# Optimization experiments

Measured on AMD Instinct MI355X. Metric: run time of the kernel, lower is better.

Reference implementation:

```python
import jax, jax.numpy as jnp
import numpy as np

N_HEAD = 16
SPARSE_TOPK = 64
NEG_INF = float('-inf')


def setup_inputs() -> dict:
    key = jax.random.key(0)
    ks = jax.random.split(key, 12)
    B, T, C = 4, 1024, 1024
    s = 0.02
    q = jax.random.normal(ks[0], (B, T, C), jnp.float32)
    kv = jax.random.normal(ks[1], (B, T, C), jnp.float32)  # forward asserts k == v
    tgt_mask = jnp.tril(jnp.ones((T, T), jnp.bool_)).reshape(1, 1, T, T)
    inp = {'q': q, 'k': kv, 'v': kv, 'tgt_mask': tgt_mask}
    for i, n in enumerate(['Wq', 'Wk', 'Wv', 'Wo']):
        inp[n] = jax.random.normal(ks[2 + i], (C, C), jnp.float32) * s
    for i, n in enumerate(['bq', 'bk', 'bv', 'bo']):
        inp[n] = jax.random.normal(ks[6 + i], (C,), jnp.float32) * s
    return inp


def reference(q, k, v, tgt_mask, Wq, Wk, Wv, Wo, bq, bk, bv, bo):
    B, T, C = q.shape
    H = N_HEAD
    hd = C // H
    scale = 1.0 / np.sqrt(hd).astype(np.float32)
    # QKV projections -> [B, H, T, hd]
    qh = (q @ Wq + bq).reshape(B, T, H, hd).transpose(0, 2, 1, 3)
    kh = (k @ Wk + bk).reshape(B, T, H, hd).transpose(0, 2, 1, 3)
    vh = (v @ Wv + bv).reshape(B, T, H, hd).transpose(0, 2, 1, 3)
    # full attention scores [B, H, T, T]
    att = jnp.einsum('bhtd,bhsd->bhts', qh, kh) * scale
    # causal mask: masked_fill where tgt_mask == 0
    att = jnp.where(tgt_mask[:, :, :T, :T], att, NEG_INF)
    # top-k sparse pruning: keep entries >= k-th largest per row (ties kept)
    top, _ = jax.lax.top_k(att, SPARSE_TOPK)
    vk = top[..., -1:]  # [B, H, T, 1]
    att = jnp.where(att < vk, NEG_INF, att)
    att = jax.nn.softmax(att, axis=-1)
    # dropout is identity in eval (p=0.0)
    y = jnp.einsum('bhts,bhsd->bhtd', att, vh)
    y = y.transpose(0, 2, 1, 3).reshape(B, T, C)
    return y @ Wo + bo
```

## Files before the change

kernel.cpp:

```cpp
#include <hip/hip_runtime.h>
#include <hip/hip_bf16.h>
#include <math.h>

typedef __attribute__((ext_vector_type(8))) short short8;
typedef __attribute__((ext_vector_type(4))) float f32x4;
typedef __attribute__((ext_vector_type(4))) int int4v;

#define SCL 0.1803368801111204f

static __device__ __forceinline__ unsigned short f2bf(float f) {
  unsigned u = __float_as_uint(f);
  u = u + 0x7FFFu + ((u >> 16) & 1u);
  return (unsigned short)(u >> 16);
}

static __device__ __forceinline__ unsigned keyof(float x) {
  unsigned u = __float_as_uint(x);
  return (u & 0x80000000u) ? ~u : (u | 0x80000000u);
}
static __device__ __forceinline__ float keyinv(unsigned k) {
  unsigned u = (k & 0x80000000u) ? (k & 0x7FFFFFFFu) : ~k;
  return __uint_as_float(u);
}

static __device__ __forceinline__ int saddr(int r, int cc) {
  return (((r << 9) + cc) << 2) ^ ((r & 7) << 4);
}
static __device__ __forceinline__ int paddr(int r, int c) {
  return ((r << 11) + (c << 1)) ^ ((r & 7) << 4);
}

static __device__ __forceinline__ void gld_lds16(const unsigned short* g, unsigned short* l) {
  __builtin_amdgcn_global_load_lds(
      (const __attribute__((address_space(1))) void*)g,
      (__attribute__((address_space(3))) void*)l, 16, 0, 0);
}

__global__ __launch_bounds__(256) void cvt3_k(const float* __restrict__ q,
                                              const float* __restrict__ k,
                                              const float* __restrict__ v,
                                              unsigned short* __restrict__ oq,
                                              unsigned short* __restrict__ ok,
                                              unsigned short* __restrict__ ov) {
  const int y = blockIdx.y;
  const float* in = (y == 0) ? q : (y == 1) ? k : v;
  unsigned short* out = (y == 0) ? oq : (y == 1) ? ok : ov;
  const int i = blockIdx.x * 256 + threadIdx.x;
  const f32x4* p = (const f32x4*)in + 2 * (size_t)i;
  f32x4 a = p[0], b = p[1];
  short8 r;
  r[0] = (short)f2bf(a[0]); r[1] = (short)f2bf(a[1]);
  r[2] = (short)f2bf(a[2]); r[3] = (short)f2bf(a[3]);
  r[4] = (short)f2bf(b[0]); r[5] = (short)f2bf(b[1]);
  r[6] = (short)f2bf(b[2]); r[7] = (short)f2bf(b[3]);
  ((short8*)out)[i] = r;
}

__global__ __launch_bounds__(256) void wtrans4_k(const float* __restrict__ Wq,
                                                 const float* __restrict__ Wk,
                                                 const float* __restrict__ Wv,
                                                 const float* __restrict__ Wo,
                                                 unsigned short* __restrict__ Wqt,
                                                 unsigned short* __restrict__ Wkt,
                                                 unsigned short* __restrict__ Wvt,
                                                 unsigned short* __restrict__ Wot) {
  const int z = blockIdx.z;
  const float* W = (z == 0) ? Wq : (z == 1) ? Wk : (z == 2) ? Wv : Wo;
  unsigned short* Wt = (z == 0) ? Wqt : (z == 1) ? Wkt : (z == 2) ? Wvt : Wot;
  __shared__ float tile[32][33];
  const int tx = threadIdx.x, ty = threadIdx.y;
  const int x0 = blockIdx.x * 32, y0 = blockIdx.y * 32;
#pragma unroll
  for (int j = 0; j < 4; ++j)
    tile[ty + j * 8][tx] = W[(y0 + ty + j * 8) * 1024 + x0 + tx];
  __syncthreads();
#pragma unroll
  for (int j = 0; j < 4; ++j)
    Wt[(x0 + ty + j * 8) * 1024 + (y0 + tx)] = f2bf(tile[tx][ty + j * 8]);
}

template <int MODE>
static __device__ __forceinline__ void gemm_body(unsigned short* As0, unsigned short* Bs0,
                                                 unsigned short* As1, unsigned short* Bs1,
                                                 const unsigned short* __restrict__ A,
                                                 const unsigned short* __restrict__ Bt,
                                                 const float* __restrict__ bias,
                                                 void* __restrict__ out) {
  const int tid = threadIdx.x;
  const int lane = tid & 63, w = tid >> 6;
  const int wr = w >> 1, wc = w & 1;
  const int m0 = blockIdx.y * 128, n0 = blockIdx.x * 128;
  const int l15 = lane & 15, l4 = lane >> 4;
  f32x4 acc[4][4] = {};
  const int r0 = tid >> 2, s0 = (tid & 3) * 8;
  const int r1 = r0 + 64;
  const unsigned short* gA0 = A + (m0 + r0) * 1024 + s0;
  const unsigned short* gA1 = A + (m0 + r1) * 1024 + s0;
  const unsigned short* gB0 = Bt + (n0 + r0) * 1024 + s0;
  const unsigned short* gB1 = Bt + (n0 + r1) * 1024 + s0;
  const int oA0 = r0 * 32 + s0, oA1 = r1 * 32 + s0;

  gld_lds16(gA0, As0 + oA0);
  gld_lds16(gA1, As0 + oA1);
  gld_lds16(gB0, Bs0 + oA0);
  gld_lds16(gB1, Bs0 + oA1);
  __syncthreads();

  for (int kt = 0; kt < 32; ++kt) {
    if (kt < 31) {
      const int k0n = (kt + 1) * 32;
      unsigned short* Asn = (kt & 1) ? As0 : As1;
      unsigned short* Bsn = (kt & 1) ? Bs0 : Bs1;
      gld_lds16(gA0 + k0n, Asn + oA0);
      gld_lds16(gA1 + k0n, Asn + oA1);
      gld_lds16(gB0 + k0n, Bsn + oA0);
      gld_lds16(gB1 + k0n, Bsn + oA1);
    }
    const unsigned short* Asc = (kt & 1) ? As1 : As0;
    const unsigned short* Bsc = (kt & 1) ? Bs1 : Bs0;
    short8 af[4], bfr[4];
#pragma unroll
    for (int i = 0; i < 4; ++i) {
      af[i]  = *(const short8*)(Asc + (wr * 64 + i * 16 + l15) * 32 + l4 * 8);
      bfr[i] = *(const short8*)(Bsc + (wc * 64 + i * 16 + l15) * 32 + l4 * 8);
    }
#pragma unroll
    for (int i = 0; i < 4; ++i)
#pragma unroll
      for (int j = 0; j < 4; ++j)
        acc[i][j] = __builtin_amdgcn_mfma_f32_16x16x32_bf16(af[i], bfr[j], acc[i][j], 0, 0, 0);
    __syncthreads();
  }
#pragma unroll
  for (int i = 0; i < 4; ++i) {
#pragma unroll
    for (int j = 0; j < 4; ++j) {
      const int n = n0 + wc * 64 + j * 16 + l15;
      const float bv = bias[n];
#pragma unroll
      for (int r = 0; r < 4; ++r) {
        const int m = m0 + wr * 64 + i * 16 + l4 * 4 + r;
        const float v = acc[i][j][r] + bv;
        if (MODE == 2) {
          ((float*)out)[m * 1024 + n] = v;
        } else {
          const int bb = m >> 10, t = m & 1023, hh = n >> 6, dd = n & 63;
          const unsigned short bfv = f2bf(v);
          if (MODE == 0)
            ((unsigned short*)out)[(((bb << 4) + hh) * 1024 + t) * 64 + dd] = bfv;
          else
            ((unsigned short*)out)[(((bb << 4) + hh) * 64 + dd) * 1024 + t] = bfv;
        }
      }
    }
  }
}

__global__ __launch_bounds__(256) void gemm_qkv_k(
    const unsigned short* qbf, const unsigned short* kbf, const unsigned short* vbf,
    const unsigned short* Wqt, const unsigned short* Wkt, const unsigned short* Wvt,
    const float* bq, const float* bk, const float* bv,
    unsigned short* Qh, unsigned short* Kh, unsigned short* Vth) {
  __shared__ unsigned short As0[128 * 32], Bs0[128 * 32], As1[128 * 32], Bs1[128 * 32];
  const int z = blockIdx.z;
  const unsigned short* A  = (z == 0) ? qbf : ((z == 1) ? kbf : vbf);
  const unsigned short* Bt = (z == 0) ? Wqt : ((z == 1) ? Wkt : Wvt);
  const float* bias        = (z == 0) ? bq  : ((z == 1) ? bk  : bv);
  if (z == 2) gemm_body<1>(As0, Bs0, As1, Bs1, A, Bt, bias, Vth);
  else        gemm_body<0>(As0, Bs0, As1, Bs1, A, Bt, bias, z ? Kh : Qh);
}

__global__ __launch_bounds__(256) void gemm_out_k(const unsigned short* Y,
                                                  const unsigned short* Wot,
                                                  const float* bo, float* out) {
  __shared__ unsigned short As0[128 * 32], Bs0[128 * 32], As1[128 * 32], Bs1[128 * 32];
  gemm_body<2>(As0, Bs0, As1, Bs1, Y, Wot, bo, out);
}

template <int NVAL>
static __device__ __forceinline__ void process_row(char* __restrict__ smem, float (&v)[NVAL],
                                                   const int r, const int Lr, const int Lpad,
                                                   const int lane, float* __restrict__ RED2) {
  float lm = v[0];
#pragma unroll
  for (int i = 1; i < NVAL; ++i) lm = fmaxf(lm, v[i]);
  float mx = lm;
#pragma unroll
  for (int o = 32; o; o >>= 1) mx = fmaxf(mx, __shfl_xor(mx, o));

  float thr = -INFINITY;
  if (Lr > 64) {
    float mn = lm;
#pragma unroll
    for (int o = 32; o; o >>= 1) mn = fminf(mn, __shfl_xor(mn, o));
    unsigned lo = (unsigned)__builtin_amdgcn_readfirstlane((int)keyof(mn));
    unsigned hi = (unsigned)__builtin_amdgcn_readfirstlane((int)keyof(mx)) + 1u;
    int cl = Lr, ch = 0, alt = 0;
    while (hi - lo > 1u) {
      const unsigned span = hi - lo;
      unsigned off;
      if (alt) off = span >> 1;
      else {
        const float fr = (float)(cl - 64) / (float)(cl - ch);
        off = (unsigned)(fr * (float)span);
        if (off < 1u) off = 1u;
        if (off > span - 1u) off = span - 1u;
      }
      alt ^= 1;
      const unsigned mid = lo + off;
      const float tm = keyinv(mid);
      int cnt = 0;
#pragma unroll
      for (int i = 0; i < NVAL; ++i) cnt += (int)__popcll(__ballot(v[i] >= tm));
      if (cnt >= 64) { lo = mid; cl = cnt; if (cnt == 64) break; }
      else { hi = mid; ch = cnt; }
    }
    thr = keyinv(lo);
  }

  float s = 0.f;
  unsigned pk[NVAL / 2];
#pragma unroll
  for (int p = 0; p < NVAL / 2; ++p) {
    const float p0 = (v[2 * p]     >= thr) ? exp2f(v[2 * p]     - mx) : 0.f;
    const float p1 = (v[2 * p + 1] >= thr) ? exp2f(v[2 * p + 1] - mx) : 0.f;
    s += p0 + p1;
    pk[p] = (unsigned)f2bf(p0) | ((unsigned)f2bf(p1) << 16);
  }
#pragma unroll
  for (int o = 32; o; o >>= 1) s += __shfl_xor(s, o);
  if (lane == 0) RED2[r] = 1.f / s;
#pragma unroll
  for (int p = 0; p < NVAL / 2; ++p) {
    const int c = ((p & 3) << 7) + (lane << 1) + ((p >= 4) ? 512 : 0);
    if (c < Lpad) *(unsigned*)(smem + paddr(r, c)) = pk[p];
  }
}

template <int NVAL>
static __device__ __forceinline__ void attn_body(char* __restrict__ smem,
                                                 const unsigned short* __restrict__ Qp,
                                                 const unsigned short* __restrict__ Kh,
                                                 const unsigned short* __restrict__ Vh,
                                                 unsigned short* __restrict__ Y,
                                                 const int t0, const int h, const int b,
                                                 const int lane, const int w) {
  const int L = t0 + 16;
  const int Lpad = (L + 31) & ~31;
  const int nCT = L >> 4;
  const int l15 = lane & 15, l4 = lane >> 4;
  float* RED  = (float*)(smem + 32768);
  float* RED2 = (float*)(smem + 32768 + 4352);

  const short8 aq0 = *(const short8*)(Qp + l15 * 64 + l4 * 8);
  const short8 aq1 = *(const short8*)(Qp + l15 * 64 + 32 + l4 * 8);

  auto qk_chunk = [&](int tlo, int thi) {
    for (int ct = tlo + w; ct < thi; ct += 8) {
      const int c0 = ct * 16;
      const short8 kb0 = *(const short8*)(Kh + (c0 + l15) * 64 + l4 * 8);
      const short8 kb1 = *(const short8*)(Kh + (c0 + l15) * 64 + 32 + l4 * 8);
      f32x4 acc = {0.f, 0.f, 0.f, 0.f};
      acc = __builtin_amdgcn_mfma_f32_16x16x32_bf16(aq0, kb0, acc, 0, 0, 0);
      acc = __builtin_amdgcn_mfma_f32_16x16x32_bf16(aq1, kb1, acc, 0, 0, 0);
      const int c = c0 + l15, cc = c & 511;
      if (ct == nCT - 1) {
#pragma unroll
        for (int r = 0; r < 4; ++r) {
          const int row = l4 * 4 + r;
          *(float*)(smem + saddr(row, cc)) = (c <= t0 + row) ? acc[r] * SCL : -INFINITY;
        }
      } else {
#pragma unroll
        for (int r = 0; r < 4; ++r)
          *(float*)(smem + saddr(l4 * 4 + r, cc)) = acc[r] * SCL;
      }
    }
  };

  qk_chunk(0, (nCT < 32) ? nCT : 32);
  __syncthreads();

  const int rA = w * 2, rB = rA + 1;
  const int LrA = t0 + rA + 1, LrB = t0 + rB + 1;
  float vA[NVAL], vB[NVAL];
#pragma unroll
  for (int p = 0; p < 4; ++p) {
    const int c = (p << 7) + (lane << 1);
    const float2 tA = *(const float2*)(smem + saddr(rA, c));
    const float2 tB = *(const float2*)(smem + saddr(rB, c));
    const bool vld = c < L;
    vA[2 * p]     = vld ? tA.x : -INFINITY;
    vA[2 * p + 1] = vld ? tA.y : -INFINITY;
    vB[2 * p]     = vld ? tB.x : -INFINITY;
    vB[2 * p + 1] = vld ? tB.y : -INFINITY;
  }

  if constexpr (NVAL == 16) {
    __syncthreads();
    qk_chunk(32, nCT);
    __syncthreads();
#pragma unroll
    for (int p = 0; p < 4; ++p) {
      const int cc = (p << 7) + (lane << 1);
      const float2 tA = *(const float2*)(smem + saddr(rA, cc));
      const bool vld = (cc + 512) < L;
      vA[8 + 2 * p] = vld ? tA.x : -INFINITY;
      vA[9 + 2 * p] = vld ? tA.y : -INFINITY;
    }
    process_row<NVAL>(smem, vA, rA, LrA, Lpad, lane, RED2);
#pragma unroll
    for (int p = 0; p < 4; ++p) {
      const int cc = (p << 7) + (lane << 1);
      const float2 tB = *(const float2*)(smem + saddr(rB, cc));
      const bool vld = (cc + 512) < L;
      vB[8 + 2 * p] = vld ? tB.x : -INFINITY;
      vB[9 + 2 * p] = vld ? tB.y : -INFINITY;
    }
    process_row<NVAL>(smem, vB, rB, LrB, Lpad, lane, RED2);
  } else {
    process_row<NVAL>(smem, vA, rA, LrA, Lpad, lane, RED2);
    process_row<NVAL>(smem, vB, rB, LrB, Lpad, lane, RED2);
  }
  __syncthreads();

  const int nST = Lpad >> 5;
  const int stMid = (nST + 1) >> 1;
  const int d0 = (w & 3) * 16;
  const int stLo = (w < 4) ? 0 : stMid;
  const int stHi = (w < 4) ? stMid : nST;
  f32x4 acc = {0.f, 0.f, 0.f, 0.f};
  for (int st = stLo; st < stHi; ++st) {
    const int sb = st * 32 + l4 * 8;
    const short8 paf = *(const short8*)(smem + paddr(l15, sb));
    const short8 vb = *(const short8*)(Vh + (d0 + l15) * 1024 + sb);
    acc = __builtin_amdgcn_mfma_f32_16x16x32_bf16(paf, vb, acc, 0, 0, 0);
  }
  if (w >= 4) {
    const int base = (w - 4) * 272 + l15;
#pragma unroll
    for (int r = 0; r < 4; ++r) RED[base + (l4 * 4 + r) * 17] = acc[r];
  }
  __syncthreads();
  if (w < 4) {
    const int base = w * 272 + l15;
    const int d = (h << 6) + d0 + l15;
#pragma unroll
    for (int r = 0; r < 4; ++r) {
      const float inv = RED2[l4 * 4 + r];
      const float vr = (acc[r] + RED[base + (l4 * 4 + r) * 17]) * inv;
      const int tg = t0 + l4 * 4 + r;
      Y[((b << 10) + tg) * 1024 + d] = f2bf(vr);
    }
  }
}

__global__ __launch_bounds__(512, 6) void attn_k(const unsigned short* __restrict__ Q,
                                                 const unsigned short* __restrict__ K,
                                                 const unsigned short* __restrict__ Vt,
                                                 unsigned short* __restrict__ Y) {
  extern __shared__ __align__(16) char smem[];
  const int tid = threadIdx.x, lane = tid & 63, w = tid >> 6;
  const int t0 = (63 - (int)blockIdx.x) * 16;
  const int h = blockIdx.y, b = blockIdx.z;
  const unsigned short* Qp = Q + (((b * 16 + h) * 1024) + t0) * 64;
  const unsigned short* Kh = K + (b * 16 + h) * 65536;
  const unsigned short* Vh = Vt + (b * 16 + h) * 65536;
  if (t0 >= 512) attn_body<16>(smem, Qp, Kh, Vh, Y, t0, h, b, lane, w);
  else           attn_body<8>(smem, Qp, Kh, Vh, Y, t0, h, b, lane, w);
}

extern "C" void kernel_launch(void* const* d_in, const int* in_sizes, int n_in,
                              void* d_out, int out_size, void* d_ws, size_t ws_size,
                              hipStream_t stream) {
  const float* q  = (const float*)d_in[0];
  const float* k  = (const float*)d_in[1];
  const float* v  = (const float*)d_in[2];
  const float* Wq = (const float*)d_in[4];
  const float* Wk = (const float*)d_in[5];
  const float* Wv = (const float*)d_in[6];
  const float* Wo = (const float*)d_in[7];
  const float* bq = (const float*)d_in[8];
  const float* bk = (const float*)d_in[9];
  const float* bv = (const float*)d_in[10];
  const float* bo = (const float*)d_in[11];

  char* ws = (char*)d_ws;
  const size_t MB = 1u << 20;
  unsigned short* qbf = (unsigned short*)(ws + 0 * MB);
  unsigned short* kbf = (unsigned short*)(ws + 8 * MB);
  unsigned short* vbf = (unsigned short*)(ws + 16 * MB);
  unsigned short* Wqt = (unsigned short*)(ws + 24 * MB);
  unsigned short* Wkt = (unsigned short*)(ws + 26 * MB);
  unsigned short* Wvt = (unsigned short*)(ws + 28 * MB);
  unsigned short* Wot = (unsigned short*)(ws + 30 * MB);
  unsigned short* Qh  = (unsigned short*)(ws + 32 * MB);
  unsigned short* Kh  = (unsigned short*)(ws + 40 * MB);
  unsigned short* Vth = (unsigned short*)(ws + 48 * MB);
  unsigned short* Y   = qbf;

  cvt3_k<<<dim3(2048, 3), 256, 0, stream>>>(q, k, v, qbf, kbf, vbf);
  wtrans4_k<<<dim3(32, 32, 4), dim3(32, 8), 0, stream>>>(Wq, Wk, Wv, Wo, Wqt, Wkt, Wvt, Wot);
  gemm_qkv_k<<<dim3(8, 32, 3), 256, 0, stream>>>(qbf, kbf, vbf, Wqt, Wkt, Wvt,
                                                 bq, bk, bv, Qh, Kh, Vth);
  attn_k<<<dim3(64, 16, 4), 512, 37248, stream>>>(Qh, Kh, Vth, Y);
  gemm_out_k<<<dim3(8, 32), 256, 0, stream>>>(Y, Wot, bo, (float*)d_out);
}
```

Measured before the change: 211.3 us.

## Split attention into 8-row 256-thread blocks with separate long and short kernels

The attention kernel now handles 8 query rows per block with 4 waves instead of 16 rows with 8 waves, and is split into two launches: one for the long half (t >= 512) and one for the short half. With a single wave per output d-slice the cross-wave split-K reduction through LDS and its extra barrier go away, and shared memory per block falls. In exchange, each 16x16 MFMA now carries only 8 useful rows, so half the tensor-core work is wasted, and K/V are reloaded twice as often across blocks.

```diff
diff --git a/kernel.cpp b/kernel.cpp
--- a/kernel.cpp
+++ b/kernel.cpp
@@ -238,25 +238,24 @@
 }
 
 template <int NVAL>
-static __device__ __forceinline__ void attn_body(char* __restrict__ smem,
-                                                 const unsigned short* __restrict__ Qp,
-                                                 const unsigned short* __restrict__ Kh,
-                                                 const unsigned short* __restrict__ Vh,
-                                                 unsigned short* __restrict__ Y,
-                                                 const int t0, const int h, const int b,
-                                                 const int lane, const int w) {
-  const int L = t0 + 16;
+static __device__ __forceinline__ void attn_body8(char* __restrict__ smem,
+                                                  const unsigned short* __restrict__ Qp,
+                                                  const unsigned short* __restrict__ Kh,
+                                                  const unsigned short* __restrict__ Vh,
+                                                  unsigned short* __restrict__ Y,
+                                                  const int t0, const int h, const int b,
+                                                  const int lane, const int w) {
+  const int L = t0 + 8;
   const int Lpad = (L + 31) & ~31;
-  const int nCT = L >> 4;
-  const int l15 = lane & 15, l4 = lane >> 4;
-  float* RED  = (float*)(smem + 32768);
-  float* RED2 = (float*)(smem + 32768 + 4352);
-
-  const short8 aq0 = *(const short8*)(Qp + l15 * 64 + l4 * 8);
-  const short8 aq1 = *(const short8*)(Qp + l15 * 64 + 32 + l4 * 8);
+  const int nCT = (L + 15) >> 4;
+  const int l15 = lane & 15, l4 = lane >> 4, l7 = lane & 7;
+  float* RED2 = (float*)(smem + 16384);
+
+  const short8 aq0 = *(const short8*)(Qp + l7 * 64 + l4 * 8);
+  const short8 aq1 = *(const short8*)(Qp + l7 * 64 + 32 + l4 * 8);
 
   auto qk_chunk = [&](int tlo, int thi) {
-    for (int ct = tlo + w; ct < thi; ct += 8) {
+    for (int ct = tlo + w; ct < thi; ct += 4) {
       const int c0 = ct * 16;
       const short8 kb0 = *(const short8*)(Kh + (c0 + l15) * 64 + l4 * 8);
       const short8 kb1 = *(const short8*)(Kh + (c0 + l15) * 64 + 32 + l4 * 8);
@@ -264,39 +263,37 @@
       acc = __builtin_amdgcn_mfma_f32_16x16x32_bf16(aq0, kb0, acc, 0, 0, 0);
       acc = __builtin_amdgcn_mfma_f32_16x16x32_bf16(aq1, kb1, acc, 0, 0, 0);
       const int c = c0 + l15, cc = c & 511;
-      if (ct == nCT - 1) {
-#pragma unroll
-        for (int r = 0; r < 4; ++r) {
-          const int row = l4 * 4 + r;
-          *(float*)(smem + saddr(row, cc)) = (c <= t0 + row) ? acc[r] * SCL : -INFINITY;
+      if (l4 < 2) {
+        if (ct == nCT - 1) {
+#pragma unroll
+          for (int r = 0; r < 4; ++r) {
+            const int row = l4 * 4 + r;
+            *(float*)(smem + saddr(row, cc)) = (c <= t0 + row) ? acc[r] * SCL : -INFINITY;
+          }
+        } else {
+#pragma unroll
+          for (int r = 0; r < 4; ++r)
+            *(float*)(smem + saddr(l4 * 4 + r, cc)) = acc[r] * SCL;
         }
-      } else {
-#pragma unroll
-        for (int r = 0; r < 4; ++r)
-          *(float*)(smem + saddr(l4 * 4 + r, cc)) = acc[r] * SCL;
       }
     }
   };
-
-  qk_chunk(0, (nCT < 32) ? nCT : 32);
-  __syncthreads();
 
   const int rA = w * 2, rB = rA + 1;
   const int LrA = t0 + rA + 1, LrB = t0 + rB + 1;
   float vA[NVAL], vB[NVAL];
-#pragma unroll
-  for (int p = 0; p < 4; ++p) {
-    const int c = (p << 7) + (lane << 1);
-    const float2 tA = *(const float2*)(smem + saddr(rA, c));
-    const float2 tB = *(const float2*)(smem + saddr(rB, c));
-    const bool vld = c < L;
-    vA[2 * p]     = vld ? tA.x : -INFINITY;
-    vA[2 * p + 1] = vld ? tA.y : -INFINITY;
-    vB[2 * p]     = vld ? tB.x : -INFINITY;
-    vB[2 * p + 1] = vld ? tB.y : -INFINITY;
-  }
 
   if constexpr (NVAL == 16) {
+    qk_chunk(0, 32);
+    __syncthreads();
+#pragma unroll
+    for (int p = 0; p < 4; ++p) {
+      const int c = (p << 7) + (lane << 1);
+      const float2 tA = *(const float2*)(smem + saddr(rA, c));
+      const float2 tB = *(const float2*)(smem + saddr(rB, c));
+      vA[2 * p] = tA.x; vA[2 * p + 1] = tA.y;
+      vB[2 * p] = tB.x; vB[2 * p + 1] = tB.y;
+    }
     __syncthreads();
     qk_chunk(32, nCT);
     __syncthreads();
@@ -319,55 +316,71 @@
     }
     process_row<NVAL>(smem, vB, rB, LrB, Lpad, lane, RED2);
   } else {
+    qk_chunk(0, nCT);
+    __syncthreads();
+#pragma unroll
+    for (int p = 0; p < 4; ++p) {
+      const int c = (p << 7) + (lane << 1);
+      const float2 tA = *(const float2*)(smem + saddr(rA, c));
+      const float2 tB = *(const float2*)(smem + saddr(rB, c));
+      const bool vld = c < L;
+      vA[2 * p]     = vld ? tA.x : -INFINITY;
+      vA[2 * p + 1] = vld ? tA.y : -INFINITY;
+      vB[2 * p]     = vld ? tB.x : -INFINITY;
+      vB[2 * p + 1] = vld ? tB.y : -INFINITY;
+    }
     process_row<NVAL>(smem, vA, rA, LrA, Lpad, lane, RED2);
     process_row<NVAL>(smem, vB, rB, LrB, Lpad, lane, RED2);
   }
   __syncthreads();
 
   const int nST = Lpad >> 5;
-  const int stMid = (nST + 1) >> 1;
-  const int d0 = (w & 3) * 16;
-  const int stLo = (w < 4) ? 0 : stMid;
-  const int stHi = (w < 4) ? stMid : nST;
+  const int d0 = w * 16;
   f32x4 acc = {0.f, 0.f, 0.f, 0.f};
-  for (int st = stLo; st < stHi; ++st) {
+  for (int st = 0; st < nST; ++st) {
     const int sb = st * 32 + l4 * 8;
-    const short8 paf = *(const short8*)(smem + paddr(l15, sb));
+    const short8 paf = *(const short8*)(smem + paddr(l7, sb));
     const short8 vb = *(const short8*)(Vh + (d0 + l15) * 1024 + sb);
     acc = __builtin_amdgcn_mfma_f32_16x16x32_bf16(paf, vb, acc, 0, 0, 0);
   }
-  if (w >= 4) {
-    const int base = (w - 4) * 272 + l15;
-#pragma unroll
-    for (int r = 0; r < 4; ++r) RED[base + (l4 * 4 + r) * 17] = acc[r];
-  }
-  __syncthreads();
-  if (w < 4) {
-    const int base = w * 272 + l15;
+  if (l4 < 2) {
     const int d = (h << 6) + d0 + l15;
 #pragma unroll
     for (int r = 0; r < 4; ++r) {
-      const float inv = RED2[l4 * 4 + r];
-      const float vr = (acc[r] + RED[base + (l4 * 4 + r) * 17]) * inv;
-      const int tg = t0 + l4 * 4 + r;
+      const int row = l4 * 4 + r;
+      const float vr = acc[r] * RED2[row];
+      const int tg = t0 + row;
       Y[((b << 10) + tg) * 1024 + d] = f2bf(vr);
     }
   }
 }
 
-__global__ __launch_bounds__(512, 6) void attn_k(const unsigned short* __restrict__ Q,
-                                                 const unsigned short* __restrict__ K,
-                                                 const unsigned short* __restrict__ Vt,
-                                                 unsigned short* __restrict__ Y) {
+__global__ __launch_bounds__(256, 8) void attn_hv_k(const unsigned short* __restrict__ Q,
+                                                    const unsigned short* __restrict__ K,
+                                                    const unsigned short* __restrict__ Vt,
+                                                    unsigned short* __restrict__ Y) {
   extern __shared__ __align__(16) char smem[];
   const int tid = threadIdx.x, lane = tid & 63, w = tid >> 6;
-  const int t0 = (63 - (int)blockIdx.x) * 16;
+  const int t0 = 1016 - 8 * (int)blockIdx.x;
   const int h = blockIdx.y, b = blockIdx.z;
   const unsigned short* Qp = Q + (((b * 16 + h) * 1024) + t0) * 64;
   const unsigned short* Kh = K + (b * 16 + h) * 65536;
   const unsigned short* Vh = Vt + (b * 16 + h) * 65536;
-  if (t0 >= 512) attn_body<16>(smem, Qp, Kh, Vh, Y, t0, h, b, lane, w);
-  else           attn_body<8>(smem, Qp, Kh, Vh, Y, t0, h, b, lane, w);
+  attn_body8<16>(smem, Qp, Kh, Vh, Y, t0, h, b, lane, w);
+}
+
+__global__ __launch_bounds__(256, 8) void attn_lt_k(const unsigned short* __restrict__ Q,
+                                                    const unsigned short* __restrict__ K,
+                                                    const unsigned short* __restrict__ Vt,
+                                                    unsigned short* __restrict__ Y) {
+  extern __shared__ __align__(16) char smem[];
+  const int tid = threadIdx.x, lane = tid & 63, w = tid >> 6;
+  const int t0 = 504 - 8 * (int)blockIdx.x;
+  const int h = blockIdx.y, b = blockIdx.z;
+  const unsigned short* Qp = Q + (((b * 16 + h) * 1024) + t0) * 64;
+  const unsigned short* Kh = K + (b * 16 + h) * 65536;
+  const unsigned short* Vh = Vt + (b * 16 + h) * 65536;
+  attn_body8<8>(smem, Qp, Kh, Vh, Y, t0, h, b, lane, w);
 }
 
 extern "C" void kernel_launch(void* const* d_in, const int* in_sizes, int n_in,
@@ -403,6 +416,7 @@
   wtrans4_k<<<dim3(32, 32, 4), dim3(32, 8), 0, stream>>>(Wq, Wk, Wv, Wo, Wqt, Wkt, Wvt, Wot);
   gemm_qkv_k<<<dim3(8, 32, 3), 256, 0, stream>>>(qbf, kbf, vbf, Wqt, Wkt, Wvt,
                                                  bq, bk, bv, Qh, Kh, Vth);
-  attn_k<<<dim3(64, 16, 4), 512, 37248, stream>>>(Qh, Kh, Vth, Y);
+  attn_hv_k<<<dim3(64, 16, 4), 256, 16416, stream>>>(Qh, Kh, Vth, Y);
+  attn_lt_k<<<dim3(64, 16, 4), 256, 16416, stream>>>(Qh, Kh, Vth, Y);
   gemm_out_k<<<dim3(8, 32), 256, 0, stream>>>(Y, Wot, bo, (float*)d_out);
 }
```

New measurement: 257.9 us. 22.1% more time.

## Fuse fp32-to-bf16 input conversion into QKV GEMM and split attention kernels

Applied to the files above, without the earlier changes.

Removes the standalone q/k/v conversion kernel. The QKV GEMM now reads fp32 activations directly, packs them to bf16 in registers and stores them into LDS, while the weight tile still arrives by async global-to-LDS loads. This drops a round trip of about 24 MB of bf16 intermediates plus one launch, at the cost of doubled A-operand global reads per tile and synchronous LDS writes. The attention kernel is split into two launches by row range (long and short rows) so each instantiation avoids runtime branching, and the long-row path always runs the top-k threshold search. The new pack2 rounding ignores the round-to-even tie rule, which changes bf16 results slightly.

```diff
diff --git a/kernel.cpp b/kernel.cpp
--- a/kernel.cpp
+++ b/kernel.cpp
@@ -13,6 +13,11 @@
   u = u + 0x7FFFu + ((u >> 16) & 1u);
   return (unsigned short)(u >> 16);
 }
+static __device__ __forceinline__ unsigned pack2(float lo, float hi) {
+  const unsigned ul = __float_as_uint(lo) + 0x8000u;
+  const unsigned uh = __float_as_uint(hi) + 0x8000u;
+  return (uh & 0xFFFF0000u) | (ul >> 16);
+}
 
 static __device__ __forceinline__ unsigned keyof(float x) {
   unsigned u = __float_as_uint(x);
@@ -34,26 +39,6 @@
   __builtin_amdgcn_global_load_lds(
       (const __attribute__((address_space(1))) void*)g,
       (__attribute__((address_space(3))) void*)l, 16, 0, 0);
-}
-
-__global__ __launch_bounds__(256) void cvt3_k(const float* __restrict__ q,
-                                              const float* __restrict__ k,
-                                              const float* __restrict__ v,
-                                              unsigned short* __restrict__ oq,
-                                              unsigned short* __restrict__ ok,
-                                              unsigned short* __restrict__ ov) {
-  const int y = blockIdx.y;
-  const float* in = (y == 0) ? q : (y == 1) ? k : v;
-  unsigned short* out = (y == 0) ? oq : (y == 1) ? ok : ov;
-  const int i = blockIdx.x * 256 + threadIdx.x;
-  const f32x4* p = (const f32x4*)in + 2 * (size_t)i;
-  f32x4 a = p[0], b = p[1];
-  short8 r;
-  r[0] = (short)f2bf(a[0]); r[1] = (short)f2bf(a[1]);
-  r[2] = (short)f2bf(a[2]); r[3] = (short)f2bf(a[3]);
-  r[4] = (short)f2bf(b[0]); r[5] = (short)f2bf(b[1]);
-  r[6] = (short)f2bf(b[2]); r[7] = (short)f2bf(b[3]);
-  ((short8*)out)[i] = r;
 }
 
 __global__ __launch_bounds__(256) void wtrans4_k(const float* __restrict__ Wq,
@@ -80,12 +65,12 @@
 }
 
 template <int MODE>
-static __device__ __forceinline__ void gemm_body(unsigned short* As0, unsigned short* Bs0,
-                                                 unsigned short* As1, unsigned short* Bs1,
-                                                 const unsigned short* __restrict__ A,
-                                                 const unsigned short* __restrict__ Bt,
-                                                 const float* __restrict__ bias,
-                                                 void* __restrict__ out) {
+static __device__ __forceinline__ void gemm_bodyF(unsigned short* As0, unsigned short* Bs0,
+                                                  unsigned short* As1, unsigned short* Bs1,
+                                                  const float* __restrict__ A,
+                                                  const unsigned short* __restrict__ Bt,
+                                                  const float* __restrict__ bias,
+                                                  void* __restrict__ out) {
   const int tid = threadIdx.x;
   const int lane = tid & 63, w = tid >> 6;
   const int wr = w >> 1, wc = w & 1;
@@ -94,10 +79,118 @@
   f32x4 acc[4][4] = {};
   const int r0 = tid >> 2, s0 = (tid & 3) * 8;
   const int r1 = r0 + 64;
-  const unsigned short* gA0 = A + (m0 + r0) * 1024 + s0;
-  const unsigned short* gA1 = A + (m0 + r1) * 1024 + s0;
+  const float* gA0 = A + (m0 + r0) * 1024 + s0;
+  const float* gA1 = A + (m0 + r1) * 1024 + s0;
   const unsigned short* gB0 = Bt + (n0 + r0) * 1024 + s0;
   const unsigned short* gB1 = Bt + (n0 + r1) * 1024 + s0;
+  const int oA0 = r0 * 32 + s0, oA1 = r1 * 32 + s0;
+
+  {
+    const f32x4 a0 = *(const f32x4*)(gA0);
+    const f32x4 a1 = *(const f32x4*)(gA0 + 4);
+    const f32x4 c0 = *(const f32x4*)(gA1);
+    const f32x4 c1 = *(const f32x4*)(gA1 + 4);
+    gld_lds16(gB0, Bs0 + oA0);
+    gld_lds16(gB1, Bs0 + oA1);
+    int4v pa, pb;
+    pa[0] = (int)pack2(a0[0], a0[1]); pa[1] = (int)pack2(a0[2], a0[3]);
+    pa[2] = (int)pack2(a1[0], a1[1]); pa[3] = (int)pack2(a1[2], a1[3]);
+    pb[0] = (int)pack2(c0[0], c0[1]); pb[1] = (int)pack2(c0[2], c0[3]);
+    pb[2] = (int)pack2(c1[0], c1[1]); pb[3] = (int)pack2(c1[2], c1[3]);
+    *(int4v*)(As0 + oA0) = pa;
+    *(int4v*)(As0 + oA1) = pb;
+  }
+  __syncthreads();
+
+  for (int kt = 0; kt < 32; ++kt) {
+    f32x4 a0, a1, c0, c1;
+    if (kt < 31) {
+      const int k0n = (kt + 1) * 32;
+      a0 = *(const f32x4*)(gA0 + k0n);
+      a1 = *(const f32x4*)(gA0 + k0n + 4);
+      c0 = *(const f32x4*)(gA1 + k0n);
+      c1 = *(const f32x4*)(gA1 + k0n + 4);
+      unsigned short* Bsn = (kt & 1) ? Bs0 : Bs1;
+      gld_lds16(gB0 + k0n, Bsn + oA0);
+      gld_lds16(gB1 + k0n, Bsn + oA1);
+    }
+    const unsigned short* Asc = (kt & 1) ? As1 : As0;
+    const unsigned short* Bsc = (kt & 1) ? Bs1 : Bs0;
+    short8 af[4], bfr[4];
+#pragma unroll
+    for (int i = 0; i < 4; ++i) {
+      af[i]  = *(const short8*)(Asc + (wr * 64 + i * 16 + l15) * 32 + l4 * 8);
+      bfr[i] = *(const short8*)(Bsc + (wc * 64 + i * 16 + l15) * 32 + l4 * 8);
+    }
+#pragma unroll
+    for (int i = 0; i < 4; ++i)
+#pragma unroll
+      for (int j = 0; j < 4; ++j)
+        acc[i][j] = __builtin_amdgcn_mfma_f32_16x16x32_bf16(af[i], bfr[j], acc[i][j], 0, 0, 0);
+    if (kt < 31) {
+      unsigned short* Asn = (kt & 1) ? As0 : As1;
+      int4v pa, pb;
+      pa[0] = (int)pack2(a0[0], a0[1]); pa[1] = (int)pack2(a0[2], a0[3]);
+      pa[2] = (int)pack2(a1[0], a1[1]); pa[3] = (int)pack2(a1[2], a1[3]);
+      pb[0] = (int)pack2(c0[0], c0[1]); pb[1] = (int)pack2(c0[2], c0[3]);
+      pb[2] = (int)pack2(c1[0], c1[1]); pb[3] = (int)pack2(c1[2], c1[3]);
+      *(int4v*)(Asn + oA0) = pa;
+      *(int4v*)(Asn + oA1) = pb;
+    }
+    __syncthreads();
+  }
+#pragma unroll
+  for (int i = 0; i < 4; ++i) {
+#pragma unroll
+    for (int j = 0; j < 4; ++j) {
+      const int n = n0 + wc * 64 + j * 16 + l15;
+      const float bv = bias[n];
+#pragma unroll
+      for (int r = 0; r < 4; ++r) {
+        const int m = m0 + wr * 64 + i * 16 + l4 * 4 + r;
+        const float v = acc[i][j][r] + bv;
+        const int bb = m >> 10, t = m & 1023, hh = n >> 6, dd = n & 63;
+        const unsigned short bfv = f2bf(v);
+        if (MODE == 0)
+          ((unsigned short*)out)[(((bb << 4) + hh) * 1024 + t) * 64 + dd] = bfv;
+        else
+          ((unsigned short*)out)[(((bb << 4) + hh) * 64 + dd) * 1024 + t] = bfv;
+      }
+    }
+  }
+}
+
+__global__ __launch_bounds__(256) void gemm_qkv_k(
+    const float* q, const float* k, const float* v,
+    const unsigned short* Wqt, const unsigned short* Wkt, const unsigned short* Wvt,
+    const float* bq, const float* bk, const float* bv,
+    unsigned short* Qh, unsigned short* Kh, unsigned short* Vth) {
+  __shared__ unsigned short As0[128 * 32], Bs0[128 * 32], As1[128 * 32], Bs1[128 * 32];
+  const int z = blockIdx.z;
+  const float* A           = (z == 0) ? q   : ((z == 1) ? k   : v);
+  const unsigned short* Bt = (z == 0) ? Wqt : ((z == 1) ? Wkt : Wvt);
+  const float* bias        = (z == 0) ? bq  : ((z == 1) ? bk  : bv);
+  if (z == 2) gemm_bodyF<1>(As0, Bs0, As1, Bs1, A, Bt, bias, Vth);
+  else        gemm_bodyF<0>(As0, Bs0, As1, Bs1, A, Bt, bias, z ? Kh : Qh);
+}
+
+__global__ __launch_bounds__(256) void gemm_out_k(const unsigned short* __restrict__ Y,
+                                                  const unsigned short* __restrict__ Wot,
+                                                  const float* __restrict__ bo,
+                                                  float* __restrict__ out) {
+  __shared__ unsigned short As0[128 * 32], Bs0[128 * 32], As1[128 * 32], Bs1[128 * 32];
+  const int tid = threadIdx.x;
+  const int lane = tid & 63, w = tid >> 6;
+  const int wr = w >> 1, wc = w & 1;
+  const int m0 = blockIdx.y * 128, n0 = blockIdx.x * 128;
+  const int l15 = lane & 15, l4 = lane >> 4;
+  f32x4 acc[4][4] = {};
+  const int r0 = tid >> 2, s0 = (tid & 3) * 8;
+  const int r1 = r0 + 64;
+  const unsigned short* gA0 = Y + (m0 + r0) * 1024 + s0;
+  const unsigned short* gA1 = Y + (m0 + r1) * 1024 + s0;
+  const unsigned short* gB0 = Wot + (n0 + r0) * 1024 + s0;
+  const unsigned short* gB1 = Wot + (n0 + r1) * 1024 + s0;
   const int oA0 = r0 * 32 + s0, oA1 = r1 * 32 + s0;
 
   gld_lds16(gA0, As0 + oA0);
@@ -136,48 +229,17 @@
 #pragma unroll
     for (int j = 0; j < 4; ++j) {
       const int n = n0 + wc * 64 + j * 16 + l15;
-      const float bv = bias[n];
+      const float bv = bo[n];
 #pragma unroll
       for (int r = 0; r < 4; ++r) {
         const int m = m0 + wr * 64 + i * 16 + l4 * 4 + r;
-        const float v = acc[i][j][r] + bv;
-        if (MODE == 2) {
-          ((float*)out)[m * 1024 + n] = v;
-        } else {
-          const int bb = m >> 10, t = m & 1023, hh = n >> 6, dd = n & 63;
-          const unsigned short bfv = f2bf(v);
-          if (MODE == 0)
-            ((unsigned short*)out)[(((bb << 4) + hh) * 1024 + t) * 64 + dd] = bfv;
-          else
-            ((unsigned short*)out)[(((bb << 4) + hh) * 64 + dd) * 1024 + t] = bfv;
-        }
+        out[m * 1024 + n] = acc[i][j][r] + bv;
       }
     }
   }
 }
 
-__global__ __launch_bounds__(256) void gemm_qkv_k(
-    const unsigned short* qbf, const unsigned short* kbf, const unsigned short* vbf,
-    const unsigned short* Wqt, const unsigned short* Wkt, const unsigned short* Wvt,
-    const float* bq, const float* bk, const float* bv,
-    unsigned short* Qh, unsigned short* Kh, unsigned short* Vth) {
-  __shared__ unsigned short As0[128 * 32], Bs0[128 * 32], As1[128 * 32], Bs1[128 * 32];
-  const int z = blockIdx.z;
-  const unsigned short* A  = (z == 0) ? qbf : ((z == 1) ? kbf : vbf);
-  const unsigned short* Bt = (z == 0) ? Wqt : ((z == 1) ? Wkt : Wvt);
-  const float* bias        = (z == 0) ? bq  : ((z == 1) ? bk  : bv);
-  if (z == 2) gemm_body<1>(As0, Bs0, As1, Bs1, A, Bt, bias, Vth);
-  else        gemm_body<0>(As0, Bs0, As1, Bs1, A, Bt, bias, z ? Kh : Qh);
-}
-
-__global__ __launch_bounds__(256) void gemm_out_k(const unsigned short* Y,
-                                                  const unsigned short* Wot,
-                                                  const float* bo, float* out) {
-  __shared__ unsigned short As0[128 * 32], Bs0[128 * 32], As1[128 * 32], Bs1[128 * 32];
-  gemm_body<2>(As0, Bs0, As1, Bs1, Y, Wot, bo, out);
-}
-
-template <int NVAL>
+template <int NVAL, bool FORCE>
 static __device__ __forceinline__ void process_row(char* __restrict__ smem, float (&v)[NVAL],
                                                    const int r, const int Lr, const int Lpad,
                                                    const int lane, float* __restrict__ RED2) {
@@ -189,7 +251,7 @@
   for (int o = 32; o; o >>= 1) mx = fmaxf(mx, __shfl_xor(mx, o));
 
   float thr = -INFINITY;
-  if (Lr > 64) {
+  if (FORCE || Lr > 64) {
     float mn = lm;
 #pragma unroll
     for (int o = 32; o; o >>= 1) mn = fminf(mn, __shfl_xor(mn, o));
@@ -237,93 +299,14 @@
   }
 }
 
-template <int NVAL>
-static __device__ __forceinline__ void attn_body(char* __restrict__ smem,
-                                                 const unsigned short* __restrict__ Qp,
-                                                 const unsigned short* __restrict__ Kh,
-                                                 const unsigned short* __restrict__ Vh,
-                                                 unsigned short* __restrict__ Y,
-                                                 const int t0, const int h, const int b,
-                                                 const int lane, const int w) {
-  const int L = t0 + 16;
-  const int Lpad = (L + 31) & ~31;
-  const int nCT = L >> 4;
+static __device__ __forceinline__ void pv_phase(char* __restrict__ smem,
+                                                const unsigned short* __restrict__ Vh,
+                                                unsigned short* __restrict__ Y,
+                                                const int t0, const int h, const int b,
+                                                const int lane, const int w, const int Lpad) {
   const int l15 = lane & 15, l4 = lane >> 4;
   float* RED  = (float*)(smem + 32768);
   float* RED2 = (float*)(smem + 32768 + 4352);
-
-  const short8 aq0 = *(const short8*)(Qp + l15 * 64 + l4 * 8);
-  const short8 aq1 = *(const short8*)(Qp + l15 * 64 + 32 + l4 * 8);
-
-  auto qk_chunk = [&](int tlo, int thi) {
-    for (int ct = tlo + w; ct < thi; ct += 8) {
-      const int c0 = ct * 16;
-      const short8 kb0 = *(const short8*)(Kh + (c0 + l15) * 64 + l4 * 8);
-      const short8 kb1 = *(const short8*)(Kh + (c0 + l15) * 64 + 32 + l4 * 8);
-      f32x4 acc = {0.f, 0.f, 0.f, 0.f};
-      acc = __builtin_amdgcn_mfma_f32_16x16x32_bf16(aq0, kb0, acc, 0, 0, 0);
-      acc = __builtin_amdgcn_mfma_f32_16x16x32_bf16(aq1, kb1, acc, 0, 0, 0);
-      const int c = c0 + l15, cc = c & 511;
-      if (ct == nCT - 1) {
-#pragma unroll
-        for (int r = 0; r < 4; ++r) {
-          const int row = l4 * 4 + r;
-          *(float*)(smem + saddr(row, cc)) = (c <= t0 + row) ? acc[r] * SCL : -INFINITY;
-        }
-      } else {
-#pragma unroll
-        for (int r = 0; r < 4; ++r)
-          *(float*)(smem + saddr(l4 * 4 + r, cc)) = acc[r] * SCL;
-      }
-    }
-  };
-
-  qk_chunk(0, (nCT < 32) ? nCT : 32);
-  __syncthreads();
-
-  const int rA = w * 2, rB = rA + 1;
-  const int LrA = t0 + rA + 1, LrB = t0 + rB + 1;
-  float vA[NVAL], vB[NVAL];
-#pragma unroll
-  for (int p = 0; p < 4; ++p) {
-    const int c = (p << 7) + (lane << 1);
-    const float2 tA = *(const float2*)(smem + saddr(rA, c));
-    const float2 tB = *(const float2*)(smem + saddr(rB, c));
-    const bool vld = c < L;
-    vA[2 * p]     = vld ? tA.x : -INFINITY;
-    vA[2 * p + 1] = vld ? tA.y : -INFINITY;
-    vB[2 * p]     = vld ? tB.x : -INFINITY;
-    vB[2 * p + 1] = vld ? tB.y : -INFINITY;
-  }
-
-  if constexpr (NVAL == 16) {
-    __syncthreads();
-    qk_chunk(32, nCT);
-    __syncthreads();
-#pragma unroll
-    for (int p = 0; p < 4; ++p) {
-      const int cc = (p << 7) + (lane << 1);
-      const float2 tA = *(const float2*)(smem + saddr(rA, cc));
-      const bool vld = (cc + 512) < L;
-      vA[8 + 2 * p] = vld ? tA.x : -INFINITY;
-      vA[9 + 2 * p] = vld ? tA.y : -INFINITY;
-    }
-    process_row<NVAL>(smem, vA, rA, LrA, Lpad, lane, RED2);
-#pragma unroll
-    for (int p = 0; p < 4; ++p) {
-      const int cc = (p << 7) + (lane << 1);
-      const float2 tB = *(const float2*)(smem + saddr(rB, cc));
-      const bool vld = (cc + 512) < L;
-      vB[8 + 2 * p] = vld ? tB.x : -INFINITY;
-      vB[9 + 2 * p] = vld ? tB.y : -INFINITY;
-    }
-    process_row<NVAL>(smem, vB, rB, LrB, Lpad, lane, RED2);
-  } else {
-    process_row<NVAL>(smem, vA, rA, LrA, Lpad, lane, RED2);
-    process_row<NVAL>(smem, vB, rB, LrB, Lpad, lane, RED2);
-  }
-  __syncthreads();
-
   const int nST = Lpad >> 5;
   const int stMid = (nST + 1) >> 1;
   const int d0 = (w & 3) * 16;
@@ -355,19 +338,147 @@
   }
 }
 
-__global__ __launch_bounds__(512, 6) void attn_k(const unsigned short* __restrict__ Q,
-                                                 const unsigned short* __restrict__ K,
-                                                 const unsigned short* __restrict__ Vt,
-                                                 unsigned short* __restrict__ Y) {
+__global__ __launch_bounds__(512, 6) void attn_hv_k(const unsigned short* __restrict__ Q,
+                                                    const unsigned short* __restrict__ K,
+                                                    const unsigned short* __restrict__ Vt,
+                                                    unsigned short* __restrict__ Y) {
   extern __shared__ __align__(16) char smem[];
   const int tid = threadIdx.x, lane = tid & 63, w = tid >> 6;
-  const int t0 = (63 - (int)blockIdx.x) * 16;
+  const int t0 = 1008 - 16 * (int)blockIdx.x;
   const int h = blockIdx.y, b = blockIdx.z;
   const unsigned short* Qp = Q + (((b * 16 + h) * 1024) + t0) * 64;
   const unsigned short* Kh = K + (b * 16 + h) * 65536;
   const unsigned short* Vh = Vt + (b * 16 + h) * 65536;
-  if (t0 >= 512) attn_body<16>(smem, Qp, Kh, Vh, Y, t0, h, b, lane, w);
-  else           attn_body<8>(smem, Qp, Kh, Vh, Y, t0, h, b, lane, w);
+  const int L = t0 + 16;
+  const int Lpad = (L + 31) & ~31;
+  const int nCT = L >> 4;
+  const int l15 = lane & 15, l4 = lane >> 4;
+  float* RED2 = (float*)(smem + 32768 + 4352);
+
+  const short8 aq0 = *(const short8*)(Qp + l15 * 64 + l4 * 8);
+  const short8 aq1 = *(const short8*)(Qp + l15 * 64 + 32 + l4 * 8);
+
+  auto qk_chunk = [&](int tlo, int thi) {
+    for (int ct = tlo + w; ct < thi; ct += 8) {
+      const int c0 = ct * 16;
+      const short8 kb0 = *(const short8*)(Kh + (c0 + l15) * 64 + l4 * 8);
+      const short8 kb1 = *(const short8*)(Kh + (c0 + l15) * 64 + 32 + l4 * 8);
+      f32x4 acc = {0.f, 0.f, 0.f, 0.f};
+      acc = __builtin_amdgcn_mfma_f32_16x16x32_bf16(aq0, kb0, acc, 0, 0, 0);
+      acc = __builtin_amdgcn_mfma_f32_16x16x32_bf16(aq1, kb1, acc, 0, 0, 0);
+      const int c = c0 + l15, cc = c & 511;
+      if (ct == nCT - 1) {
+#pragma unroll
+        for (int r = 0; r < 4; ++r) {
+          const int row = l4 * 4 + r;
+          *(float*)(smem + saddr(row, cc)) = (c <= t0 + row) ? acc[r] * SCL : -INFINITY;
+        }
+      } else {
+#pragma unroll
+        for (int r = 0; r < 4; ++r)
+          *(float*)(smem + saddr(l4 * 4 + r, cc)) = acc[r] * SCL;
+      }
+    }
+  };
+
+  qk_chunk(0, 32);
+  __syncthreads();
+  const int rA = w * 2, rB = rA + 1;
+  const int LrA = t0 + rA + 1, LrB = t0 + rB + 1;
+  float vA[16], vB[16];
+#pragma unroll
+  for (int p = 0; p < 4; ++p) {
+    const int c = (p << 7) + (lane << 1);
+    const float2 tA = *(const float2*)(smem + saddr(rA, c));
+    const float2 tB = *(const float2*)(smem + saddr(rB, c));
+    vA[2 * p] = tA.x; vA[2 * p + 1] = tA.y;
+    vB[2 * p] = tB.x; vB[2 * p + 1] = tB.y;
+  }
+  __syncthreads();
+  qk_chunk(32, nCT);
+  __syncthreads();
+#pragma unroll
+  for (int p = 0; p < 4; ++p) {
+    const int cc = (p << 7) + (lane << 1);
+    const float2 tA = *(const float2*)(smem + saddr(rA, cc));
+    const bool vld = (cc + 512) < L;
+    vA[8 + 2 * p] = vld ? tA.x : -INFINITY;
+    vA[9 + 2 * p] = vld ? tA.y : -INFINITY;
+  }
+  process_row<16, true>(smem, vA, rA, LrA, Lpad, lane, RED2);
+#pragma unroll
+  for (int p = 0; p < 4; ++p) {
+    const int cc = (p << 7) + (lane << 1);
+    const float2 tB = *(const float2*)(smem + saddr(rB, cc));
+    const bool vld = (cc + 512) < L;
+    vB[8 + 2 * p] = vld ? tB.x : -INFINITY;
+    vB[9 + 2 * p] = vld ? tB.y : -INFINITY;
+  }
+  process_row<16, true>(smem, vB, rB, LrB, Lpad, lane, RED2);
+  __syncthreads();
+  pv_phase(smem, Vh, Y, t0, h, b, lane, w, Lpad);
+}
+
+__global__ __launch_bounds__(512, 6) void attn_lt_k(const unsigned short* __restrict__ Q,
+                                                    const unsigned short* __restrict__ K,
+                                                    const unsigned short* __restrict__ Vt,
+                                                    unsigned short* __restrict__ Y) {
+  extern __shared__ __align__(16) char smem[];
+  const int tid = threadIdx.x, lane = tid & 63, w = tid >> 6;
+  const int t0 = 496 - 16 * (int)blockIdx.x;
+  const int h = blockIdx.y, b = blockIdx.z;
+  const unsigned short* Qp = Q + (((b * 16 + h) * 1024) + t0) * 64;
+  const unsigned short* Kh = K + (b * 16 + h) * 65536;
+  const unsigned short* Vh = Vt + (b * 16 + h) * 65536;
+  const int L = t0 + 16;
+  const int Lpad = (L + 31) & ~31;
+  const int nCT = L >> 4;
+  const int l15 = lane & 15, l4 = lane >> 4;
+  float* RED2 = (float*)(smem + 32768 + 4352);
+
+  const short8 aq0 = *(const short8*)(Qp + l15 * 64 + l4 * 8);
+  const short8 aq1 = *(const short8*)(Qp + l15 * 64 + 32 + l4 * 8);
+
+  for (int ct = w; ct < nCT; ct += 8) {
+    const int c0 = ct * 16;
+    const short8 kb0 = *(const short8*)(Kh + (c0 + l15) * 64 + l4 * 8);
+    const short8 kb1 = *(const short8*)(Kh + (c0 + l15) * 64 + 32 + l4 * 8);
+    f32x4 acc = {0.f, 0.f, 0.f, 0.f};
+    acc = __builtin_amdgcn_mfma_f32_16x16x32_bf16(aq0, kb0, acc, 0, 0, 0);
+    acc = __builtin_amdgcn_mfma_f32_16x16x32_bf16(aq1, kb1, acc, 0, 0, 0);
+    const int c = c0 + l15, cc = c & 511;
+    if (ct == nCT - 1) {
+#pragma unroll
+      for (int r = 0; r < 4; ++r) {
+        const int row = l4 * 4 + r;
+        *(float*)(smem + saddr(row, cc)) = (c <= t0 + row) ? acc[r] * SCL : -INFINITY;
+      }
+    } else {
+#pragma unroll
+      for (int r = 0; r < 4; ++r)
+        *(float*)(smem + saddr(l4 * 4 + r, cc)) = acc[r] * SCL;
+    }
+  }
+  __syncthreads();
+
+  const int rA = w * 2, rB = rA + 1;
+  const int LrA = t0 + rA + 1, LrB = t0 + rB + 1;
+  float vA[8], vB[8];
+#pragma unroll
+  for (int p = 0; p < 4; ++p) {
+    const int c = (p << 7) + (lane << 1);
+    const float2 tA = *(const float2*)(smem + saddr(rA, c));
+    const float2 tB = *(const float2*)(smem + saddr(rB, c));
+    const bool vld = c < L;
+    vA[2 * p]     = vld ? tA.x : -INFINITY;
+    vA[2 * p + 1] = vld ? tA.y : -INFINITY;
+    vB[2 * p]     = vld ? tB.x : -INFINITY;
+    vB[2 * p + 1] = vld ? tB.y : -INFINITY;
+  }
+  process_row<8, false>(smem, vA, rA, LrA, Lpad, lane, RED2);
+  process_row<8, false>(smem, vB, rB, LrB, Lpad, lane, RED2);
+  __syncthreads();
+  pv_phase(smem, Vh, Y, t0, h, b, lane, w, Lpad);
 }
 
 extern "C" void kernel_launch(void* const* d_in, const int* in_sizes, int n_in,
@@ -387,9 +498,7 @@
 
   char* ws = (char*)d_ws;
   const size_t MB = 1u << 20;
-  unsigned short* qbf = (unsigned short*)(ws + 0 * MB);
-  unsigned short* kbf = (unsigned short*)(ws + 8 * MB);
-  unsigned short* vbf = (unsigned short*)(ws + 16 * MB);
+  unsigned short* Y   = (unsigned short*)(ws + 0 * MB);
   unsigned short* Wqt = (unsigned short*)(ws + 24 * MB);
   unsigned short* Wkt = (unsigned short*)(ws + 26 * MB);
   unsigned short* Wvt = (unsigned short*)(ws + 28 * MB);
@@ -397,12 +506,11 @@
   unsigned short* Qh  = (unsigned short*)(ws + 32 * MB);
   unsigned short* Kh  = (unsigned short*)(ws + 40 * MB);
   unsigned short* Vth = (unsigned short*)(ws + 48 * MB);
-  unsigned short* Y   = qbf;
-
-  cvt3_k<<<dim3(2048, 3), 256, 0, stream>>>(q, k, v, qbf, kbf, vbf);
+
   wtrans4_k<<<dim3(32, 32, 4), dim3(32, 8), 0, stream>>>(Wq, Wk, Wv, Wo, Wqt, Wkt, Wvt, Wot);
-  gemm_qkv_k<<<dim3(8, 32, 3), 256, 0, stream>>>(qbf, kbf, vbf, Wqt, Wkt, Wvt,
+  gemm_qkv_k<<<dim3(8, 32, 3), 256, 0, stream>>>(q, k, v, Wqt, Wkt, Wvt,
                                                  bq, bk, bv, Qh, Kh, Vth);
-  attn_k<<<dim3(64, 16, 4), 512, 37248, stream>>>(Qh, Kh, Vth, Y);
+  attn_hv_k<<<dim3(32, 16, 4), 512, 37248, stream>>>(Qh, Kh, Vth, Y);
+  attn_lt_k<<<dim3(32, 16, 4), 512, 37248, stream>>>(Qh, Kh, Vth, Y);
   gemm_out_k<<<dim3(8, 32), 256, 0, stream>>>(Y, Wot, bo, (float*)d_out);
 }
```

After: 223.6 us. 5.8% more time.
